# Optimization experiments

Hardware: AMD Instinct MI355X
Metric: run time of the kernel (lower is better)

Reference implementation:

```python
import jax, jax.numpy as jnp
import numpy as np

B, T, D = 2, 2048, 2048
H, KV, DH = 16, 8, 128
N, W, K = 1024, 256, 8


def rotate_half(x):
    x1, x2 = x[..., : DH // 2], x[..., DH // 2 :]
    return jnp.concatenate((-x2, x1), axis=-1)


def setup_inputs() -> dict:
    key = jax.random.key(0)
    ks = jax.random.split(key, 10)
    hidden_states = jax.random.normal(ks[0], (B, T, D), dtype=jnp.float32)
    cos = jax.random.uniform(ks[1], (B, T, DH), dtype=jnp.float32, minval=-1.0, maxval=1.0)
    sin = jax.random.uniform(ks[2], (B, T, DH), dtype=jnp.float32, minval=-1.0, maxval=1.0)
    mem = jax.random.normal(ks[3], (B, N, D), dtype=jnp.float32)
    Wq = jax.random.normal(ks[4], (D, D), dtype=jnp.float32) * 0.02
    Wk = jax.random.normal(ks[5], (KV * DH, D), dtype=jnp.float32) * 0.02
    Wv = jax.random.normal(ks[6], (KV * DH, D), dtype=jnp.float32) * 0.02
    Wo = jax.random.normal(ks[7], (D, D), dtype=jnp.float32) * 0.02
    Wg = jnp.zeros((1, D), dtype=jnp.float32)          # module inits gate weight to zeros
    bg = jnp.full((1,), 2.0, dtype=jnp.float32)        # and gate bias to 2.0
    return dict(hidden_states=hidden_states, cos=cos, sin=sin, mem=mem,
                Wq=Wq, Wk=Wk, Wv=Wv, Wo=Wo, Wg=Wg, bg=bg)


def reference(hidden_states, cos, sin, mem, Wq, Wk, Wv, Wo, Wg, bg):
    scale = DH ** -0.5
    n_rep = H // KV
    # projections -> [B, heads, T, d_h]
    q = (hidden_states @ Wq.T).reshape(B, T, H, DH).transpose(0, 2, 1, 3)
    k = (hidden_states @ Wk.T).reshape(B, T, KV, DH).transpose(0, 2, 1, 3)
    v = (hidden_states @ Wv.T).reshape(B, T, KV, DH).transpose(0, 2, 1, 3)
    # rotary (cos/sin are [B,T,d_h] -> broadcast over heads)
    c, s = cos[:, None], sin[:, None]
    q = q * c + rotate_half(q) * s
    k = k * c + rotate_half(k) * s
    # GQA repeat kv heads
    k_local = jnp.repeat(k, n_rep, axis=1)
    v_local = jnp.repeat(v, n_rep, axis=1)
    # --- local sliding-window causal attention (dense TxT mask, as in SDPA path) ---
    row = jnp.arange(T)[:, None]
    col = jnp.arange(T)[None, :]
    allowed = (col <= row) & (col >= row - W + 1)
    bias = jnp.where(allowed, 0.0, -jnp.inf).astype(q.dtype)
    scores = jnp.einsum('bhtd,bhsd->bhts', q, k_local) * scale + bias
    o_local = jnp.einsum('bhts,bhsd->bhtd', jax.nn.softmax(scores, axis=-1), v_local)
    o_local = o_local.transpose(0, 2, 1, 3).reshape(B, T, D) @ Wo.T
    # --- memory retrieval path (memory is detached in the original) ---
    mem_c = jax.lax.stop_gradient(mem)
    k_mem = (mem_c @ Wk.T).reshape(B, N, KV, DH).transpose(0, 2, 1, 3)
    v_mem = (mem_c @ Wv.T).reshape(B, N, KV, DH).transpose(0, 2, 1, 3)
    k_mem = jnp.repeat(k_mem, n_rep, axis=1)  # [B,H,N,d_h]
    v_mem = jnp.repeat(v_mem, n_rep, axis=1)
    q_chunk = q.mean(axis=2)                  # [B,H,d_h]
    sim_chunk = jnp.einsum('bhd,bhnd->bhn', q_chunk, k_mem) * scale
    _, idx = jax.lax.top_k(sim_chunk, K)      # [B,H,K]
    k_sh = jnp.take_along_axis(k_mem, idx[..., None], axis=2)  # [B,H,K,d_h]
    v_sh = jnp.take_along_axis(v_mem, idx[..., None], axis=2)
    sim_tok = jnp.einsum('bhtd,bhkd->bhtk', q, k_sh) * scale
    o_mem = jnp.einsum('bhtk,bhkd->bhtd', jax.nn.softmax(sim_tok, axis=-1), v_sh)
    o_mem = o_mem.transpose(0, 2, 1, 3).reshape(B, T, D)
    # --- learned gate fusion ---
    g = jax.nn.sigmoid(hidden_states @ Wg.T + bg)  # [B,T,1]
    return g * o_local + (1.0 - g) * o_mem
```

## Files before the change

### kernel.cpp

```cpp
#include <hip/hip_runtime.h>
#include <stdint.h>

#define B_   2
#define T_   2048
#define D_   2048
#define H_   16
#define KV_  8
#define DH_  128
#define NMEM 1024
#define WWIN 256
#define KSEL 8
#define BT   (B_*T_)
#define KVSTR 2048
#define QKVSTR 4096

__constant__ const float kScale = 0.08838834764831845f;

typedef __attribute__((ext_vector_type(8))) short s16x8;
typedef __attribute__((ext_vector_type(4))) float f32x4;

__device__ inline unsigned short f2bf(float f) {
  union { float f; unsigned int u; } c; c.f = f;
  unsigned int u = c.u;
  unsigned int r = u + 0x7fffu + ((u >> 16) & 1u);
  return (unsigned short)(r >> 16);
}
__device__ inline float bf2f(unsigned short v) {
  union { unsigned int u; float f; } c; c.u = ((unsigned int)v) << 16;
  return c.f;
}
__device__ inline f32x4 fzero4() { f32x4 v; v[0]=0.f; v[1]=0.f; v[2]=0.f; v[3]=0.f; return v; }

__global__ __launch_bounds__(256) void conv_kernel(const float* __restrict__ src,
                                                   unsigned short* __restrict__ dst, int n) {
  int i = blockIdx.x * 256 + threadIdx.x;
  if (i * 4 >= n) return;
  float4 v = ((const float4*)src)[i];
  uint2 o;
  o.x = (unsigned)f2bf(v.x) | ((unsigned)f2bf(v.y) << 16);
  o.y = (unsigned)f2bf(v.z) | ((unsigned)f2bf(v.w) << 16);
  ((uint2*)dst)[i] = o;
}

#define AOFF(buf, half) ((buf)*32768 + (half)*16384)
#define BOFF(buf, half) (65536 + (buf)*32768 + (half)*16384)

#define PH_MFMA(P, BF) \
  { \
    _Pragma("unroll") \
    for (int mi = 0; mi < 2; ++mi) { \
      _Pragma("unroll") \
      for (int ni = 0; ni < 4; ++ni) { \
        acc[P][mi][ni] = __builtin_amdgcn_mfma_f32_16x16x32_bf16(af[mi][0], BF[ni][0], acc[P][mi][ni], 0, 0, 0); \
        acc[P][mi][ni] = __builtin_amdgcn_mfma_f32_16x16x32_bf16(af[mi][1], BF[ni][1], acc[P][mi][ni], 0, 0, 0); \
      } \
    } \
  }

template<int MODE>
__global__ __launch_bounds__(512, 2) void gemm256(const unsigned short* __restrict__ A,
                                                  const unsigned short* __restrict__ Bw,
                                                  int N, int K, int lda, int ldc,
                                                  unsigned short* __restrict__ Cb,
                                                  const float* __restrict__ g,
                                                  const unsigned short* __restrict__ omem,
                                                  float* __restrict__ dout) {
  __shared__ __align__(16) char lds[131072];
  const int tid = threadIdx.x;
  const int wv = tid >> 6, lane = tid & 63;
  const int l15 = lane & 15, lg = lane >> 4;
  const int wr = wv >> 1, wc = wv & 1;
  const int gx = gridDim.x;
  const int nwg = gx * gridDim.y;
  const int flat = blockIdx.y * gx + blockIdx.x;
  const int chunk = nwg >> 3;
  const int wg = (flat & 7) * chunk + (flat >> 3);
  const int bx = wg % gx, by = wg / gx;
  const int m0 = by * 256, n0 = bx * 256;
  const int NT = K >> 6;

  auto stage_half = [&](const unsigned short* base, int stride, int row0, int koff, int ldsoff) {
#pragma unroll
    for (int ld = 0; ld < 2; ++ld) {
      int s = ld * 512 + tid;
      int row = s >> 3, cs = s & 7;
      int cg = cs ^ (row & 7);
      const unsigned short* src = base + (size_t)(row0 + row) * stride + koff + cg * 8;
      __builtin_amdgcn_global_load_lds((const __attribute__((address_space(1))) void*)src,
          (__attribute__((address_space(3))) void*)(lds + ldsoff + ld * 8192 + wv * 1024), 16, 0, 0);
    }
  };
  auto rdA = [&](int buf, int half, int mi, int kk) -> s16x8 {
    int r = wr * 32 + mi * 16 + l15;
    int slot = (kk * 4 + lg) ^ (r & 7);
    return *(const s16x8*)(lds + AOFF(buf, half) + r * 128 + slot * 16);
  };
  auto rdB = [&](int buf, int half, int ni, int kk) -> s16x8 {
    int r = wc * 64 + ni * 16 + l15;
    int slot = (kk * 4 + lg) ^ (r & 7);
    return *(const s16x8*)(lds + BOFF(buf, half) + r * 128 + slot * 16);
  };

  f32x4 acc[4][2][4];
#pragma unroll
  for (int p = 0; p < 4; ++p)
#pragma unroll
    for (int mi = 0; mi < 2; ++mi)
#pragma unroll
      for (int ni = 0; ni < 4; ++ni) acc[p][mi][ni] = fzero4();

  stage_half(A,  lda, m0,       0,  AOFF(0, 0));
  stage_half(Bw, K,   n0,       0,  BOFF(0, 0));
  stage_half(A,  lda, m0 + 128, 0,  AOFF(0, 1));
  stage_half(Bw, K,   n0 + 128, 0,  BOFF(0, 1));
  stage_half(A,  lda, m0,       64, AOFF(1, 0));
  stage_half(Bw, K,   n0,       64, BOFF(1, 0));
  stage_half(A,  lda, m0 + 128, 64, AOFF(1, 1));
  asm volatile("s_waitcnt vmcnt(6)" ::: "memory");
  __builtin_amdgcn_s_barrier();

  int cur = 0;
  for (int t = 0; t < NT; ++t, cur ^= 1) {
    const int nxt = cur ^ 1;
    s16x8 af[2][2], b0f[4][2], b1f[4][2];
#pragma unroll
    for (int mi = 0; mi < 2; ++mi) {
      af[mi][0] = rdA(cur, 0, mi, 0);
      af[mi][1] = rdA(cur, 0, mi, 1);
    }
#pragma unroll
    for (int ni = 0; ni < 4; ++ni) {
      b0f[ni][0] = rdB(cur, 0, ni, 0);
      b0f[ni][1] = rdB(cur, 0, ni, 1);
    }
    if (t + 1 < NT) stage_half(Bw, K, n0 + 128, (t + 1) * 64, BOFF(nxt, 1));
    __builtin_amdgcn_sched_barrier(0);
    __builtin_amdgcn_s_barrier();
    asm volatile("s_waitcnt lgkmcnt(0)" ::: "memory");
    __builtin_amdgcn_sched_barrier(0);
    __builtin_amdgcn_s_setprio(1);
    PH_MFMA(0, b0f);
    __builtin_amdgcn_s_setprio(0);
    __builtin_amdgcn_s_barrier();
#pragma unroll
    for (int ni = 0; ni < 4; ++ni) {
      b1f[ni][0] = rdB(cur, 1, ni, 0);
      b1f[ni][1] = rdB(cur, 1, ni, 1);
    }
    if (t + 2 < NT) stage_half(A, lda, m0, (t + 2) * 64, AOFF(cur, 0));
    __builtin_amdgcn_sched_barrier(0);
    __builtin_amdgcn_s_barrier();
    asm volatile("s_waitcnt lgkmcnt(0)" ::: "memory");
    __builtin_amdgcn_sched_barrier(0);
    __builtin_amdgcn_s_setprio(1);
    PH_MFMA(1, b1f);
    __builtin_amdgcn_s_setprio(0);
    __builtin_amdgcn_s_barrier();
#pragma unroll
    for (int mi = 0; mi < 2; ++mi) {
      af[mi][0] = rdA(cur, 1, mi, 0);
      af[mi][1] = rdA(cur, 1, mi, 1);
    }
    if (t + 2 < NT) stage_half(Bw, K, n0, (t + 2) * 64, BOFF(cur, 0));
    __builtin_amdgcn_sched_barrier(0);
    __builtin_amdgcn_s_barrier();
    asm volatile("s_waitcnt lgkmcnt(0)" ::: "memory");
    __builtin_amdgcn_sched_barrier(0);
    __builtin_amdgcn_s_setprio(1);
    PH_MFMA(2, b0f);
    __builtin_amdgcn_s_setprio(0);
    __builtin_amdgcn_s_barrier();
    if (t + 2 < NT) stage_half(A, lda, m0 + 128, (t + 2) * 64, AOFF(cur, 1));
    __builtin_amdgcn_sched_barrier(0);
    __builtin_amdgcn_s_barrier();
    __builtin_amdgcn_s_setprio(1);
    PH_MFMA(3, b1f);
    __builtin_amdgcn_s_setprio(0);
    if (t < NT - 2) asm volatile("s_waitcnt vmcnt(6)" ::: "memory");
    else            asm volatile("s_waitcnt vmcnt(0)" ::: "memory");
    __builtin_amdgcn_s_barrier();
  }

#pragma unroll
  for (int p = 0; p < 4; ++p)
#pragma unroll
    for (int mi = 0; mi < 2; ++mi)
#pragma unroll
      for (int ni = 0; ni < 4; ++ni)
#pragma unroll
        for (int j = 0; j < 4; ++j) {
          int row_g = m0 + (p >> 1) * 128 + wr * 32 + mi * 16 + lg * 4 + j;
          int col_g = n0 + (p & 1) * 128 + wc * 64 + ni * 16 + l15;
          float v = acc[p][mi][ni][j];
          size_t o = (size_t)row_g * ldc + col_g;
          if constexpr (MODE == 0) {
            Cb[o] = f2bf(v);
          } else {
            float gv = g[row_g];
            dout[o] = gv * v + (1.f - gv) * bf2f(omem[o]);
          }
        }
}

template<int MODE>
__global__ __launch_bounds__(256) void gemm_bt(const unsigned short* __restrict__ A,
                                               const unsigned short* __restrict__ Bw,
                                               int N, int K, int lda, int ldc,
                                               unsigned short* __restrict__ Cb,
                                               const float* __restrict__ g,
                                               const unsigned short* __restrict__ omem,
                                               float* __restrict__ dout) {
  __shared__ __align__(16) unsigned short sA[128 * 32];
  __shared__ __align__(16) unsigned short sB[128 * 32];
  const int tid = threadIdx.x;
  const int wv = tid >> 6, lane = tid & 63;
  const int gx = gridDim.x;
  const int nwg = gx * gridDim.y;
  const int flat = blockIdx.y * gx + blockIdx.x;
  const int chunk = nwg >> 3;
  const int wg = (flat & 7) * chunk + (flat >> 3);
  const int bx = wg % gx, by = wg / gx;
  const int m0 = by * 128, n0 = bx * 128;
  const int wr = wv >> 1, wc = wv & 1;
  const int l15 = lane & 15, lg = lane >> 4;
  const int rowA = tid >> 2;
  const int colB = (tid & 3) * 16;
  f32x4 acc[4][4];
#pragma unroll
  for (int mi = 0; mi < 4; ++mi)
#pragma unroll
    for (int ni = 0; ni < 4; ++ni) acc[mi][ni] = fzero4();

  char* sAc = (char*)sA;
  char* sBc = (char*)sB;
  for (int k0 = 0; k0 < K; k0 += 32) {
#pragma unroll
    for (int e = 0; e < 2; ++e) {
      const char* ga = (const char*)(A + ((size_t)(m0 + rowA + e * 64) * lda + k0)) + colB;
      __builtin_amdgcn_global_load_lds((const __attribute__((address_space(1))) void*)ga,
          (__attribute__((address_space(3))) void*)(sAc + e * 4096 + wv * 1024), 16, 0, 0);
      const char* gb = (const char*)(Bw + ((size_t)(n0 + rowA + e * 64) * K + k0)) + colB;
      __builtin_amdgcn_global_load_lds((const __attribute__((address_space(1))) void*)gb,
          (__attribute__((address_space(3))) void*)(sBc + e * 4096 + wv * 1024), 16, 0, 0);
    }
    __syncthreads();
    s16x8 af[4], bf_[4];
#pragma unroll
    for (int mi = 0; mi < 4; ++mi)
      af[mi] = *(const s16x8*)&sA[(wr * 64 + mi * 16 + l15) * 32 + lg * 8];
#pragma unroll
    for (int ni = 0; ni < 4; ++ni)
      bf_[ni] = *(const s16x8*)&sB[(wc * 64 + ni * 16 + l15) * 32 + lg * 8];
#pragma unroll
    for (int mi = 0; mi < 4; ++mi)
#pragma unroll
      for (int ni = 0; ni < 4; ++ni)
        acc[mi][ni] = __builtin_amdgcn_mfma_f32_16x16x32_bf16(af[mi], bf_[ni], acc[mi][ni], 0, 0, 0);
    __syncthreads();
  }
#pragma unroll
  for (int mi = 0; mi < 4; ++mi)
#pragma unroll
    for (int ni = 0; ni < 4; ++ni)
#pragma unroll
      for (int j = 0; j < 4; ++j) {
        int row_g = m0 + wr * 64 + mi * 16 + lg * 4 + j;
        int col_g = n0 + wc * 64 + ni * 16 + l15;
        float v = acc[mi][ni][j];
        size_t o = (size_t)row_g * ldc + col_g;
        if constexpr (MODE == 0) {
          Cb[o] = f2bf(v);
        } else {
          float gv = g[row_g];
          float om = bf2f(omem[o]);
          dout[o] = gv * v + (1.f - gv) * om;
        }
      }
}

__global__ __launch_bounds__(256) void rope_ip_kernel(unsigned short* __restrict__ buf,
                                                      const float* __restrict__ cosp,
                                                      const float* __restrict__ sinp,
                                                      int logp, int stride, int nthreads) {
  int i = blockIdx.x * 256 + threadIdx.x;
  if (i >= nthreads) return;
  int pp = i * 8;
  int row = pp >> logp;
  int p0 = pp & ((1 << logp) - 1);
  int blk = p0 >> 6, dd0 = p0 & 63;
  int b = row >> 11, t = row & 2047;
  const float* cb = cosp + ((size_t)b * T_ + t) * DH_;
  const float* sb = sinp + ((size_t)b * T_ + t) * DH_;
  unsigned short* p1 = buf + (size_t)row * stride + blk * 128 + dd0;
  s16x8 a = *(s16x8*)p1;
  s16x8 b8 = *(s16x8*)(p1 + 64);
  s16x8 o1, o2;
#pragma unroll
  for (int e = 0; e < 8; ++e) {
    float c1 = cb[dd0 + e], s1 = sb[dd0 + e];
    float c2 = cb[dd0 + 64 + e], s2 = sb[dd0 + 64 + e];
    float x1 = bf2f((unsigned short)a[e]), x2 = bf2f((unsigned short)b8[e]);
    o1[e] = (short)f2bf(x1 * c1 - x2 * s1);
    o2[e] = (short)f2bf(x2 * c2 + x1 * s2);
  }
  *(s16x8*)p1 = o1;
  *(s16x8*)(p1 + 64) = o2;
}

__global__ __launch_bounds__(256) void cs_kernel(const float* __restrict__ hs,
                                                 const float* __restrict__ cosp,
                                                 const float* __restrict__ sinp,
                                                 float* __restrict__ Cp, float* __restrict__ Sp) {
  __shared__ __align__(16) float hsL[32][128];
  __shared__ __align__(16) float csL[32][32];
  __shared__ __align__(16) float snL[32][32];
  const int tid = threadIdx.x;
  const int j0 = blockIdx.x * 128, d0 = blockIdx.y * 32;
  const int b = blockIdx.z >> 3, sp = blockIdx.z & 7;
  const int dq = (tid & 7) * 4;
  const int jq = (tid >> 3) * 4;
  float4 aC[4], aS[4];
#pragma unroll
  for (int a = 0; a < 4; ++a) {
    aC[a] = make_float4(0.f, 0.f, 0.f, 0.f);
    aS[a] = make_float4(0.f, 0.f, 0.f, 0.f);
  }
  const int csrow = tid >> 3, csc4 = tid & 7;
  for (int tile = 0; tile < 8; ++tile) {
    int t0 = sp * 256 + tile * 32;
    const float4* hs4 = (const float4*)(hs + ((size_t)b * T_ + t0) * D_ + j0);
#pragma unroll
    for (int r = 0; r < 4; ++r) {
      int i = tid + r * 256;
      int row = i >> 5, c4 = i & 31;
      *(float4*)&hsL[row][c4 * 4] = hs4[(size_t)row * (D_ / 4) + c4];
    }
    const float4* cp4 = (const float4*)(cosp + ((size_t)b * T_ + t0) * DH_ + d0);
    const float4* sp4 = (const float4*)(sinp + ((size_t)b * T_ + t0) * DH_ + d0);
    *(float4*)&csL[csrow][csc4 * 4] = cp4[(size_t)csrow * (DH_ / 4) + csc4];
    *(float4*)&snL[csrow][csc4 * 4] = sp4[(size_t)csrow * (DH_ / 4) + csc4];
    __syncthreads();
#pragma unroll 8
    for (int tt = 0; tt < 32; ++tt) {
      float4 cv = *(const float4*)&csL[tt][dq];
      float4 sv = *(const float4*)&snL[tt][dq];
      float4 hv = *(const float4*)&hsL[tt][jq];
      float ca[4] = {cv.x, cv.y, cv.z, cv.w};
      float sa[4] = {sv.x, sv.y, sv.z, sv.w};
#pragma unroll
      for (int a = 0; a < 4; ++a) {
        aC[a].x += ca[a] * hv.x; aC[a].y += ca[a] * hv.y;
        aC[a].z += ca[a] * hv.z; aC[a].w += ca[a] * hv.w;
        aS[a].x += sa[a] * hv.x; aS[a].y += sa[a] * hv.y;
        aS[a].z += sa[a] * hv.z; aS[a].w += sa[a] * hv.w;
      }
    }
    __syncthreads();
  }
#pragma unroll
  for (int a = 0; a < 4; ++a) {
    size_t o = ((size_t)(sp * B_ + b) * DH_ + d0 + dq + a) * D_ + j0 + jq;
    *(float4*)&Cp[o] = aC[a];
    *(float4*)&Sp[o] = aS[a];
  }
}

__global__ __launch_bounds__(256) void reduce_cs_kernel(const float4* __restrict__ Cp,
                                                        const float4* __restrict__ Sp,
                                                        float4* __restrict__ Cr,
                                                        float4* __restrict__ Sr) {
  int i = blockIdx.x * 256 + threadIdx.x;
  const int str = (B_ * DH_ * D_) / 4;
  float4 c = Cp[i], s = Sp[i];
#pragma unroll
  for (int p = 1; p < 8; ++p) {
    float4 cp = Cp[i + (size_t)p * str], sq = Sp[i + (size_t)p * str];
    c.x += cp.x; c.y += cp.y; c.z += cp.z; c.w += cp.w;
    s.x += sq.x; s.y += sq.y; s.z += sq.z; s.w += sq.w;
  }
  Cr[i] = c; Sr[i] = s;
}

__global__ __launch_bounds__(256) void qchunk_kernel(const float* __restrict__ Wq,
                                                     const float* __restrict__ Cr,
                                                     const float* __restrict__ Sr,
                                                     float* __restrict__ qc) {
  int gid = blockIdx.x * 256 + threadIdx.x;
  int wid = gid >> 6, lane = gid & 63;
  int b = wid >> 11, rem = wid & 2047;
  int h = rem >> 7, d = rem & 127;
  const float* w1 = Wq + (size_t)(h * DH_ + d) * D_;
  int dp = (d < 64) ? d + 64 : d - 64;
  float sgn = (d < 64) ? -1.f : 1.f;
  const float* w2 = Wq + (size_t)(h * DH_ + dp) * D_;
  const float* crow = Cr + ((size_t)b * DH_ + d) * D_;
  const float* srow = Sr + ((size_t)b * DH_ + d) * D_;
  float a1 = 0.f, a2 = 0.f;
  for (int j = lane; j < D_; j += 64) { a1 += w1[j] * crow[j]; a2 += w2[j] * srow[j]; }
#pragma unroll
  for (int off = 1; off < 64; off <<= 1) { a1 += __shfl_xor(a1, off); a2 += __shfl_xor(a2, off); }
  if (lane == 0) qc[wid] = (a1 + sgn * a2) * (1.f / (float)T_);
}

__global__ __launch_bounds__(256) void zk_kernel(const float* __restrict__ qc,
                                                 const float* __restrict__ Wk,
                                                 float* __restrict__ z) {
  int j = blockIdx.x * 256 + threadIdx.x;
  int h = blockIdx.y, b = blockIdx.z;
  int kvh = h >> 1;
  const float* qcl = qc + ((size_t)b * H_ + h) * DH_;
  const float* wb = Wk + (size_t)kvh * DH_ * D_ + j;
  float acc = 0.f;
#pragma unroll 8
  for (int d = 0; d < 128; ++d) acc += qcl[d] * wb[(size_t)d * D_];
  z[((size_t)b * H_ + h) * D_ + j] = acc;
}

__global__ __launch_bounds__(256) void sim_kernel(const float* __restrict__ z,
                                                  const float* __restrict__ mem,
                                                  float* __restrict__ sim) {
  __shared__ float4 mL[16 * 512];
  int tid = threadIdx.x;
  int n0 = blockIdx.x * 16, b = blockIdx.y;
  const float4* mem4 = (const float4*)(mem + (size_t)b * NMEM * D_);
#pragma unroll
  for (int c = 0; c < 32; ++c) {
    int i = tid + c * 256;
    int r = i >> 9, j4 = i & 511;
    mL[r * 512 + (j4 ^ (r & 7))] = mem4[(size_t)(n0 + r) * 512 + j4];
  }
  __syncthreads();
  int h = tid >> 4, n = tid & 15;
  const float4* zr = (const float4*)(z + ((size_t)b * H_ + h) * D_);
  float acc = 0.f;
  for (int j4 = 0; j4 < 512; ++j4) {
    float4 zz = zr[j4];
    float4 mm = mL[n * 512 + (j4 ^ (n & 7))];
    acc += zz.x * mm.x + zz.y * mm.y + zz.z * mm.z + zz.w * mm.w;
  }
  sim[((size_t)b * H_ + h) * NMEM + n0 + n] = acc * kScale;
}

__global__ __launch_bounds__(256) void topk_kernel(const float* __restrict__ sim,
                                                   int* __restrict__ idx) {
  __shared__ float sL[1024];
  __shared__ float rv[256];
  __shared__ int ri[256];
  int tid = threadIdx.x;
  int h = blockIdx.x, b = blockIdx.y;
  const float* sp = sim + ((size_t)b * H_ + h) * NMEM;
#pragma unroll
  for (int r = 0; r < 4; ++r) sL[tid + r * 256] = sp[tid + r * 256];
  __syncthreads();
  for (int kk = 0; kk < 8; ++kk) {
    float bv = -INFINITY; int bi = 0x7fffffff;
#pragma unroll
    for (int r = 0; r < 4; ++r) {
      int i = tid + r * 256;
      float v = sL[i];
      if (v > bv || (v == bv && i < bi)) { bv = v; bi = i; }
    }
    rv[tid] = bv; ri[tid] = bi;
    __syncthreads();
    for (int s = 128; s > 0; s >>= 1) {
      if (tid < s) {
        float v2 = rv[tid + s]; int i2 = ri[tid + s];
        if (v2 > rv[tid] || (v2 == rv[tid] && i2 < ri[tid])) { rv[tid] = v2; ri[tid] = i2; }
      }
      __syncthreads();
    }
    if (tid == 0) { idx[((size_t)b * H_ + h) * KSEL + kk] = ri[0]; sL[ri[0]] = -INFINITY; }
    __syncthreads();
  }
}

__global__ __launch_bounds__(256) void memattn_kernel(const unsigned short* __restrict__ qbf,
                                                      const unsigned short* __restrict__ kvmem,
                                                      const int* __restrict__ idx,
                                                      unsigned short* __restrict__ omem) {
  __shared__ float kl[8][128];
  __shared__ float vl[8][128];
  __shared__ int selL[8];
  int tid = threadIdx.x;
  int b = blockIdx.z, h = blockIdx.y, t = blockIdx.x * 256 + tid;
  int kvh = h >> 1;
  if (tid < 8) selL[tid] = idx[((size_t)b * H_ + h) * KSEL + tid];
  __syncthreads();
  {
    int r = tid >> 5, c4 = (tid & 31) * 4;
    size_t rb = ((size_t)b * NMEM + selL[r]) * (size_t)KVSTR;
    ushort4 k4 = *(const ushort4*)(kvmem + rb + kvh * DH_ + c4);
    ushort4 v4 = *(const ushort4*)(kvmem + rb + KV_ * DH_ + kvh * DH_ + c4);
    kl[r][c4 + 0] = bf2f(k4.x); kl[r][c4 + 1] = bf2f(k4.y);
    kl[r][c4 + 2] = bf2f(k4.z); kl[r][c4 + 3] = bf2f(k4.w);
    vl[r][c4 + 0] = bf2f(v4.x); vl[r][c4 + 1] = bf2f(v4.y);
    vl[r][c4 + 2] = bf2f(v4.z); vl[r][c4 + 3] = bf2f(v4.w);
  }
  __syncthreads();
  float sc[8] = {0.f,0.f,0.f,0.f,0.f,0.f,0.f,0.f};
  const unsigned short* qr = qbf + (size_t)(b * T_ + t) * QKVSTR + h * DH_;
  for (int c = 0; c < 4; ++c) {
    const s16x8* qp = (const s16x8*)(qr + c * 32);
#pragma unroll
    for (int u = 0; u < 4; ++u) {
      s16x8 q8 = qp[u];
#pragma unroll
      for (int e = 0; e < 8; ++e) {
        float qv = bf2f((unsigned short)q8[e]);
        int d = c * 32 + u * 8 + e;
#pragma unroll
        for (int kk = 0; kk < 8; ++kk) sc[kk] += qv * kl[kk][d];
      }
    }
  }
  float sm[8], mx = -INFINITY;
#pragma unroll
  for (int kk = 0; kk < 8; ++kk) { sm[kk] = sc[kk] * kScale; mx = fmaxf(mx, sm[kk]); }
  float sum = 0.f;
#pragma unroll
  for (int kk = 0; kk < 8; ++kk) { sm[kk] = __expf(sm[kk] - mx); sum += sm[kk]; }
  float inv = 1.f / sum;
#pragma unroll
  for (int kk = 0; kk < 8; ++kk) sm[kk] *= inv;
  unsigned short* orow = omem + (size_t)(b * T_ + t) * D_ + h * DH_;
  for (int d = 0; d < 128; d += 4) {
    float o0 = 0.f, o1 = 0.f, o2 = 0.f, o3 = 0.f;
#pragma unroll
    for (int kk = 0; kk < 8; ++kk) {
      float w = sm[kk];
      o0 += w * vl[kk][d + 0];
      o1 += w * vl[kk][d + 1];
      o2 += w * vl[kk][d + 2];
      o3 += w * vl[kk][d + 3];
    }
    uint2 pk;
    pk.x = (unsigned)f2bf(o0) | ((unsigned)f2bf(o1) << 16);
    pk.y = (unsigned)f2bf(o2) | ((unsigned)f2bf(o3) << 16);
    *(uint2*)(orow + d) = pk;
  }
}

__global__ __launch_bounds__(256) void gate_kernel(const float* __restrict__ hs,
                                                   const float* __restrict__ Wg,
                                                   const float* __restrict__ bg,
                                                   float* __restrict__ g) {
  int gid = blockIdx.x * 256 + threadIdx.x;
  int row = gid >> 6, lane = gid & 63;
  const float4* hr = (const float4*)(hs + (size_t)row * D_);
  const float4* wg4 = (const float4*)Wg;
  float acc = 0.f;
#pragma unroll
  for (int it = 0; it < 8; ++it) {
    float4 hv = hr[lane + it * 64], wv = wg4[lane + it * 64];
    acc += hv.x * wv.x + hv.y * wv.y + hv.z * wv.z + hv.w * wv.w;
  }
#pragma unroll
  for (int off = 1; off < 64; off <<= 1) acc += __shfl_xor(acc, off);
  if (lane == 0) g[row] = 1.f / (1.f + __expf(-(acc + bg[0])));
}

__global__ __launch_bounds__(256) void localattn_kernel(const unsigned short* __restrict__ qbf,
                                                        const unsigned short* __restrict__ kbf,
                                                        const unsigned short* __restrict__ vbf,
                                                        unsigned short* __restrict__ olocal) {
  __shared__ __align__(16) unsigned short kL[2][32][128];
  __shared__ __align__(16) unsigned short vL[2][128][32];
  __shared__ __align__(16) unsigned short pl[4][16][40];
  const int tid = threadIdx.x;
  const int w = tid >> 6, lane = tid & 63;
  const int tb = blockIdx.x * 64;
  const int h = blockIdx.y, b = blockIdx.z;
  const int kvh = h >> 1;
  const int t0 = tb + w * 16;
  const int l15 = lane & 15, lg = lane >> 4;

  s16x8 qf[4];
  {
    const unsigned short* qb = qbf + ((size_t)(b * T_ + t0 + l15) * QKVSTR) + h * DH_ + lg * 8;
#pragma unroll
    for (int kb = 0; kb < 4; ++kb) qf[kb] = *(const s16x8*)(qb + kb * 32);
  }
  f32x4 of[8];
#pragma unroll
  for (int nb = 0; nb < 8; ++nb) of[nb] = fzero4();
  float m_r[4] = {-INFINITY, -INFINITY, -INFINITY, -INFINITY};
  float l_r[4] = {0.f, 0.f, 0.f, 0.f};

  int sstart = tb - (WWIN - 1);
  if (sstart < 0) sstart = 0;
  sstart &= ~31;
  const int slast = tb + 63;

  const int vk = tid & 15, vcg = tid >> 4;
  auto STAGE = [&](int buf, int s0) {
#pragma unroll
    for (int ld = 0; ld < 2; ++ld) {
      int s = ld * 256 + tid;
      int r = s >> 4, cs = s & 15;
      int cg = cs ^ (r & 7);
      const unsigned short* src = kbf + (size_t)(b * T_ + s0 + r) * QKVSTR + kvh * DH_ + cg * 8;
      __builtin_amdgcn_global_load_lds((const __attribute__((address_space(1))) void*)src,
          (__attribute__((address_space(3))) void*)((char*)&kL[buf][0][0] + ld * 4096 + w * 1024), 16, 0, 0);
    }
    {
      int r0 = 2 * vk;
      const unsigned short* vs = vbf + (size_t)(b * T_ + s0 + r0) * QKVSTR + kvh * DH_ + vcg * 8;
      s16x8 va = *(const s16x8*)vs;
      s16x8 vb2 = *(const s16x8*)(vs + QKVSTR);
      int q = vk >> 2;
      int colbase = 2 * (vk & 3);
#pragma unroll
      for (int e = 0; e < 8; ++e) {
        int c = vcg * 8 + e;
        int blk = q ^ ((c >> 2) & 3);
        unsigned int val = (unsigned int)(unsigned short)va[e] |
                           ((unsigned int)(unsigned short)vb2[e] << 16);
        *(unsigned int*)&vL[buf][c][blk * 8 + colbase] = val;
      }
    }
  };

  STAGE(0, sstart);
  int buf = 0;
  const int vp = (l15 >> 2) & 3;
  for (int s0 = sstart; s0 <= slast; s0 += 32, buf ^= 1) {
    __syncthreads();
    if (s0 + 32 <= slast) STAGE(buf ^ 1, s0 + 32);

    f32x4 sc[2];
    sc[0] = fzero4(); sc[1] = fzero4();
#pragma unroll
    for (int cb = 0; cb < 2; ++cb) {
#pragma unroll
      for (int kb = 0; kb < 4; ++kb) {
        int r = cb * 16 + l15;
        int c = kb * 4 + lg;
        s16x8 kf = *(const s16x8*)((char*)&kL[buf][0][0] + r * 256 + ((c ^ (r & 7)) * 16));
        sc[cb] = __builtin_amdgcn_mfma_f32_16x16x32_bf16(qf[kb], kf, sc[cb], 0, 0, 0);
      }
    }
    float pv[2][4];
#pragma unroll
    for (int j = 0; j < 4; ++j) {
      int t = t0 + lg * 4 + j;
      int s_a = s0 + l15, s_b = s_a + 16;
      float va = sc[0][j] * kScale;
      float vb = sc[1][j] * kScale;
      va = (s_a <= t && s_a + (WWIN - 1) >= t) ? va : -INFINITY;
      vb = (s_b <= t && s_b + (WWIN - 1) >= t) ? vb : -INFINITY;
      float mx = fmaxf(va, vb);
#pragma unroll
      for (int off = 1; off < 16; off <<= 1) mx = fmaxf(mx, __shfl_xor(mx, off));
      float mn = fmaxf(m_r[j], mx);
      float alpha, pa, pb;
      if (mn == -INFINITY) { alpha = 1.f; pa = 0.f; pb = 0.f; }
      else {
        alpha = __expf(m_r[j] - mn);
        pa = __expf(va - mn);
        pb = __expf(vb - mn);
      }
      m_r[j] = mn;
      float rs = pa + pb;
#pragma unroll
      for (int off = 1; off < 16; off <<= 1) rs += __shfl_xor(rs, off);
      l_r[j] = l_r[j] * alpha + rs;
#pragma unroll
      for (int nb = 0; nb < 8; ++nb) of[nb][j] *= alpha;
      pv[0][j] = pa; pv[1][j] = pb;
    }
#pragma unroll
    for (int cb = 0; cb < 2; ++cb)
#pragma unroll
      for (int j = 0; j < 4; ++j)
        pl[w][lg * 4 + j][cb * 16 + l15] = f2bf(pv[cb][j]);
    asm volatile("s_waitcnt lgkmcnt(0)" ::: "memory");
    __builtin_amdgcn_sched_barrier(0);
    s16x8 pa8 = *(const s16x8*)&pl[w][l15][lg * 8];
#pragma unroll
    for (int nb = 0; nb < 8; ++nb) {
      int c = nb * 16 + l15;
      s16x8 vf = *(const s16x8*)&vL[buf][c][(lg ^ vp) * 8];
      of[nb] = __builtin_amdgcn_mfma_f32_16x16x32_bf16(pa8, vf, of[nb], 0, 0, 0);
    }
  }

  float inv[4];
#pragma unroll
  for (int j = 0; j < 4; ++j) inv[j] = 1.f / l_r[j];
#pragma unroll
  for (int nb = 0; nb < 8; ++nb)
#pragma unroll
    for (int j = 0; j < 4; ++j) {
      int t = t0 + lg * 4 + j;
      olocal[(size_t)(b * T_ + t) * QKVSTR + h * DH_ + nb * 16 + l15] = f2bf(of[nb][j] * inv[j]);
    }
}

extern "C" void kernel_launch(void* const* d_in, const int* in_sizes, int n_in,
                              void* d_out, int out_size, void* d_ws, size_t ws_size,
                              hipStream_t stream) {
  const float* hs   = (const float*)d_in[0];
  const float* cosp = (const float*)d_in[1];
  const float* sinp = (const float*)d_in[2];
  const float* mem  = (const float*)d_in[3];
  const float* Wq   = (const float*)d_in[4];
  const float* Wk   = (const float*)d_in[5];
  const float* Wv   = (const float*)d_in[6];
  const float* Wo   = (const float*)d_in[7];
  const float* Wg   = (const float*)d_in[8];
  const float* bg   = (const float*)d_in[9];
  float* out = (float*)d_out;

  char* p = (char*)d_ws;
  auto alloc = [&](size_t bytes) { char* r = p; p += (bytes + 255) & ~(size_t)255; return r; };
  float* qc     = (float*)alloc((size_t)B_ * H_ * DH_ * 4);
  float* gbuf   = (float*)alloc((size_t)BT * 4);
  float* zbuf   = (float*)alloc((size_t)B_ * H_ * D_ * 4);
  float* simbuf = (float*)alloc((size_t)B_ * H_ * NMEM * 4);
  int*   idxbuf = (int*)alloc((size_t)B_ * H_ * KSEL * 4);
  unsigned short* hs_bf   = (unsigned short*)alloc((size_t)BT * D_ * 2);
  unsigned short* qkv_raw = (unsigned short*)alloc((size_t)BT * QKVSTR * 2);
  unsigned short* wbig    = (unsigned short*)alloc((size_t)2 * D_ * D_ * 2);
  unsigned short* mem_bf  = (unsigned short*)alloc((size_t)B_ * NMEM * D_ * 2);
  unsigned short* kvmem   = (unsigned short*)alloc((size_t)B_ * NMEM * KVSTR * 2);

  float* Cp = (float*)d_out;
  float* Sp = Cp + (size_t)8 * B_ * DH_ * D_;
  float* Cr = (float*)mem_bf;
  float* Sr = Cr + (size_t)B_ * DH_ * D_;
  unsigned short* omem_bf = hs_bf;

  conv_kernel<<<(BT * D_ / 4 + 255) / 256, 256, 0, stream>>>(hs, hs_bf, BT * D_);
  conv_kernel<<<(D_ * D_ / 4 + 255) / 256, 256, 0, stream>>>(Wq, wbig, D_ * D_);
  conv_kernel<<<(KV_ * DH_ * D_ / 4 + 255) / 256, 256, 0, stream>>>(Wk, wbig + (size_t)D_ * D_, KV_ * DH_ * D_);
  conv_kernel<<<(KV_ * DH_ * D_ / 4 + 255) / 256, 256, 0, stream>>>(Wv, wbig + (size_t)D_ * D_ + (size_t)KV_ * DH_ * D_, KV_ * DH_ * D_);
  gemm256<0><<<dim3(QKVSTR / 256, BT / 256), 512, 0, stream>>>(hs_bf, wbig, QKVSTR, D_, D_, QKVSTR, qkv_raw, nullptr, nullptr, nullptr);
  conv_kernel<<<(B_ * NMEM * D_ / 4 + 255) / 256, 256, 0, stream>>>(mem, mem_bf, B_ * NMEM * D_);
  gemm_bt<0><<<dim3(KVSTR / 128, (B_ * NMEM) / 128), 256, 0, stream>>>(mem_bf, wbig + (size_t)D_ * D_, KVSTR, D_, D_, KVSTR, kvmem, nullptr, nullptr, nullptr);

  rope_ip_kernel<<<(BT * D_ / 16 + 255) / 256, 256, 0, stream>>>(qkv_raw, cosp, sinp, 10, QKVSTR, BT * D_ / 16);
  rope_ip_kernel<<<(BT * KV_ * DH_ / 16 + 255) / 256, 256, 0, stream>>>(qkv_raw + D_, cosp, sinp, 9, QKVSTR, BT * KV_ * DH_ / 16);

  cs_kernel<<<dim3(D_ / 128, DH_ / 32, B_ * 8), 256, 0, stream>>>(hs, cosp, sinp, Cp, Sp);
  reduce_cs_kernel<<<(B_ * DH_ * D_ / 4) / 256, 256, 0, stream>>>((const float4*)Cp, (const float4*)Sp, (float4*)Cr, (float4*)Sr);
  qchunk_kernel<<<(B_ * H_ * DH_) / 4, 256, 0, stream>>>(Wq, Cr, Sr, qc);
  zk_kernel<<<dim3(D_ / 256, H_, B_), 256, 0, stream>>>(qc, Wk, zbuf);
  sim_kernel<<<dim3(NMEM / 16, B_), 256, 0, stream>>>(zbuf, mem, simbuf);
  topk_kernel<<<dim3(H_, B_), 256, 0, stream>>>(simbuf, idxbuf);

  memattn_kernel<<<dim3(T_ / 256, H_, B_), 256, 0, stream>>>(qkv_raw, kvmem, idxbuf, omem_bf);

  gate_kernel<<<BT / 4, 256, 0, stream>>>(hs, Wg, bg, gbuf);

  localattn_kernel<<<dim3(T_ / 64, H_, B_), 256, 0, stream>>>(qkv_raw, qkv_raw + D_, qkv_raw + D_ + KV_ * DH_, qkv_raw);

  conv_kernel<<<(D_ * D_ / 4 + 255) / 256, 256, 0, stream>>>(Wo, wbig, D_ * D_);
  gemm256<1><<<dim3(D_ / 256, BT / 256), 512, 0, stream>>>(qkv_raw, wbig, D_, D_, QKVSTR, D_, nullptr, gbuf, omem_bf, out);
}
```

Baseline: 437.2 us.

## Merge memory K/V projection into the main QKV GEMM via stacked rows

Stacks the bf16 hidden states and memory rows into one A buffer and runs a single 256-tile GEMM producing Q, K and V for both, removing the separate 128-tile gemm_bt launch for memory K/V. Memory attention now reads selected K/V rows from the combined output buffer. This removes one kernel launch and uses the larger-tile GEMM for the memory projection, but computes an unneeded Q projection for memory rows, adding GEMM work and output traffic.

```diff
diff --git a/kernel.cpp b/kernel.cpp
--- a/kernel.cpp
+++ b/kernel.cpp
@@ -11,8 +11,8 @@
 #define WWIN 256
 #define KSEL 8
 #define BT   (B_*T_)
-#define KVSTR 2048
 #define QKVSTR 4096
+#define MROWS (BT + B_*NMEM)
 
 __constant__ const float kScale = 0.08838834764831845f;
 
@@ -202,82 +202,6 @@
         }
 }
 
-template<int MODE>
-__global__ __launch_bounds__(256) void gemm_bt(const unsigned short* __restrict__ A,
-                                               const unsigned short* __restrict__ Bw,
-                                               int N, int K, int lda, int ldc,
-                                               unsigned short* __restrict__ Cb,
-                                               const float* __restrict__ g,
-                                               const unsigned short* __restrict__ omem,
-                                               float* __restrict__ dout) {
-  __shared__ __align__(16) unsigned short sA[128 * 32];
-  __shared__ __align__(16) unsigned short sB[128 * 32];
-  const int tid = threadIdx.x;
-  const int wv = tid >> 6, lane = tid & 63;
-  const int gx = gridDim.x;
-  const int nwg = gx * gridDim.y;
-  const int flat = blockIdx.y * gx + blockIdx.x;
-  const int chunk = nwg >> 3;
-  const int wg = (flat & 7) * chunk + (flat >> 3);
-  const int bx = wg % gx, by = wg / gx;
-  const int m0 = by * 128, n0 = bx * 128;
-  const int wr = wv >> 1, wc = wv & 1;
-  const int l15 = lane & 15, lg = lane >> 4;
-  const int rowA = tid >> 2;
-  const int colB = (tid & 3) * 16;
-  f32x4 acc[4][4];
-#pragma unroll
-  for (int mi = 0; mi < 4; ++mi)
-#pragma unroll
-    for (int ni = 0; ni < 4; ++ni) acc[mi][ni] = fzero4();
-
-  char* sAc = (char*)sA;
-  char* sBc = (char*)sB;
-  for (int k0 = 0; k0 < K; k0 += 32) {
-#pragma unroll
-    for (int e = 0; e < 2; ++e) {
-      const char* ga = (const char*)(A + ((size_t)(m0 + rowA + e * 64) * lda + k0)) + colB;
-      __builtin_amdgcn_global_load_lds((const __attribute__((address_space(1))) void*)ga,
-          (__attribute__((address_space(3))) void*)(sAc + e * 4096 + wv * 1024), 16, 0, 0);
-      const char* gb = (const char*)(Bw + ((size_t)(n0 + rowA + e * 64) * K + k0)) + colB;
-      __builtin_amdgcn_global_load_lds((const __attribute__((address_space(1))) void*)gb,
-          (__attribute__((address_space(3))) void*)(sBc + e * 4096 + wv * 1024), 16, 0, 0);
-    }
-    __syncthreads();
-    s16x8 af[4], bf_[4];
-#pragma unroll
-    for (int mi = 0; mi < 4; ++mi)
-      af[mi] = *(const s16x8*)&sA[(wr * 64 + mi * 16 + l15) * 32 + lg * 8];
-#pragma unroll
-    for (int ni = 0; ni < 4; ++ni)
-      bf_[ni] = *(const s16x8*)&sB[(wc * 64 + ni * 16 + l15) * 32 + lg * 8];
-#pragma unroll
-    for (int mi = 0; mi < 4; ++mi)
-#pragma unroll
-      for (int ni = 0; ni < 4; ++ni)
-        acc[mi][ni] = __builtin_amdgcn_mfma_f32_16x16x32_bf16(af[mi], bf_[ni], acc[mi][ni], 0, 0, 0);
-    __syncthreads();
-  }
-#pragma unroll
-  for (int mi = 0; mi < 4; ++mi)
-#pragma unroll
-    for (int ni = 0; ni < 4; ++ni)
-#pragma unroll
-      for (int j = 0; j < 4; ++j) {
-        int row_g = m0 + wr * 64 + mi * 16 + lg * 4 + j;
-        int col_g = n0 + wc * 64 + ni * 16 + l15;
-        float v = acc[mi][ni][j];
-        size_t o = (size_t)row_g * ldc + col_g;
-        if constexpr (MODE == 0) {
-          Cb[o] = f2bf(v);
-        } else {
-          float gv = g[row_g];
-          float om = bf2f(omem[o]);
-          dout[o] = gv * v + (1.f - gv) * om;
-        }
-      }
-}
-
 __global__ __launch_bounds__(256) void rope_ip_kernel(unsigned short* __restrict__ buf,
                                                       const float* __restrict__ cosp,
                                                       const float* __restrict__ sinp,
@@ -475,7 +399,7 @@
 }
 
 __global__ __launch_bounds__(256) void memattn_kernel(const unsigned short* __restrict__ qbf,
-                                                      const unsigned short* __restrict__ kvmem,
+                                                      const unsigned short* __restrict__ qkvm,
                                                       const int* __restrict__ idx,
                                                       unsigned short* __restrict__ omem) {
   __shared__ float kl[8][128];
@@ -488,9 +412,9 @@
   __syncthreads();
   {
     int r = tid >> 5, c4 = (tid & 31) * 4;
-    size_t rb = ((size_t)b * NMEM + selL[r]) * (size_t)KVSTR;
-    ushort4 k4 = *(const ushort4*)(kvmem + rb + kvh * DH_ + c4);
-    ushort4 v4 = *(const ushort4*)(kvmem + rb + KV_ * DH_ + kvh * DH_ + c4);
+    size_t rb = ((size_t)(BT + b * NMEM + selL[r])) * (size_t)QKVSTR;
+    ushort4 k4 = *(const ushort4*)(qkvm + rb + D_ + kvh * DH_ + c4);
+    ushort4 v4 = *(const ushort4*)(qkvm + rb + D_ + KV_ * DH_ + kvh * DH_ + c4);
     kl[r][c4 + 0] = bf2f(k4.x); kl[r][c4 + 1] = bf2f(k4.y);
     kl[r][c4 + 2] = bf2f(k4.z); kl[r][c4 + 3] = bf2f(k4.w);
     vl[r][c4 + 0] = bf2f(v4.x); vl[r][c4 + 1] = bf2f(v4.y);
@@ -718,28 +642,27 @@
   float* zbuf   = (float*)alloc((size_t)B_ * H_ * D_ * 4);
   float* simbuf = (float*)alloc((size_t)B_ * H_ * NMEM * 4);
   int*   idxbuf = (int*)alloc((size_t)B_ * H_ * KSEL * 4);
-  unsigned short* hs_bf   = (unsigned short*)alloc((size_t)BT * D_ * 2);
-  unsigned short* qkv_raw = (unsigned short*)alloc((size_t)BT * QKVSTR * 2);
-  unsigned short* wbig    = (unsigned short*)alloc((size_t)2 * D_ * D_ * 2);
-  unsigned short* mem_bf  = (unsigned short*)alloc((size_t)B_ * NMEM * D_ * 2);
-  unsigned short* kvmem   = (unsigned short*)alloc((size_t)B_ * NMEM * KVSTR * 2);
-
+  unsigned short* Abuf  = (unsigned short*)alloc((size_t)MROWS * D_ * 2);
+  unsigned short* qkvm  = (unsigned short*)alloc((size_t)MROWS * QKVSTR * 2);
+  unsigned short* wbig  = (unsigned short*)alloc((size_t)2 * D_ * D_ * 2);
+
+  unsigned short* hs_bf  = Abuf;
+  unsigned short* mem_bf = Abuf + (size_t)BT * D_;
   float* Cp = (float*)d_out;
   float* Sp = Cp + (size_t)8 * B_ * DH_ * D_;
-  float* Cr = (float*)mem_bf;
+  float* Cr = (float*)Abuf;
   float* Sr = Cr + (size_t)B_ * DH_ * D_;
-  unsigned short* omem_bf = hs_bf;
+  unsigned short* omem_bf = Abuf;
 
   conv_kernel<<<(BT * D_ / 4 + 255) / 256, 256, 0, stream>>>(hs, hs_bf, BT * D_);
+  conv_kernel<<<(B_ * NMEM * D_ / 4 + 255) / 256, 256, 0, stream>>>(mem, mem_bf, B_ * NMEM * D_);
   conv_kernel<<<(D_ * D_ / 4 + 255) / 256, 256, 0, stream>>>(Wq, wbig, D_ * D_);
   conv_kernel<<<(KV_ * DH_ * D_ / 4 + 255) / 256, 256, 0, stream>>>(Wk, wbig + (size_t)D_ * D_, KV_ * DH_ * D_);
   conv_kernel<<<(KV_ * DH_ * D_ / 4 + 255) / 256, 256, 0, stream>>>(Wv, wbig + (size_t)D_ * D_ + (size_t)KV_ * DH_ * D_, KV_ * DH_ * D_);
-  gemm256<0><<<dim3(QKVSTR / 256, BT / 256), 512, 0, stream>>>(hs_bf, wbig, QKVSTR, D_, D_, QKVSTR, qkv_raw, nullptr, nullptr, nullptr);
-  conv_kernel<<<(B_ * NMEM * D_ / 4 + 255) / 256, 256, 0, stream>>>(mem, mem_bf, B_ * NMEM * D_);
-  gemm_bt<0><<<dim3(KVSTR / 128, (B_ * NMEM) / 128), 256, 0, stream>>>(mem_bf, wbig + (size_t)D_ * D_, KVSTR, D_, D_, KVSTR, kvmem, nullptr, nullptr, nullptr);
-
-  rope_ip_kernel<<<(BT * D_ / 16 + 255) / 256, 256, 0, stream>>>(qkv_raw, cosp, sinp, 10, QKVSTR, BT * D_ / 16);
-  rope_ip_kernel<<<(BT * KV_ * DH_ / 16 + 255) / 256, 256, 0, stream>>>(qkv_raw + D_, cosp, sinp, 9, QKVSTR, BT * KV_ * DH_ / 16);
+  gemm256<0><<<dim3(QKVSTR / 256, MROWS / 256), 512, 0, stream>>>(Abuf, wbig, QKVSTR, D_, D_, QKVSTR, qkvm, nullptr, nullptr, nullptr);
+
+  rope_ip_kernel<<<(BT * D_ / 16 + 255) / 256, 256, 0, stream>>>(qkvm, cosp, sinp, 10, QKVSTR, BT * D_ / 16);
+  rope_ip_kernel<<<(BT * KV_ * DH_ / 16 + 255) / 256, 256, 0, stream>>>(qkvm + D_, cosp, sinp, 9, QKVSTR, BT * KV_ * DH_ / 16);
 
   cs_kernel<<<dim3(D_ / 128, DH_ / 32, B_ * 8), 256, 0, stream>>>(hs, cosp, sinp, Cp, Sp);
   reduce_cs_kernel<<<(B_ * DH_ * D_ / 4) / 256, 256, 0, stream>>>((const float4*)Cp, (const float4*)Sp, (float4*)Cr, (float4*)Sr);
@@ -748,12 +671,12 @@
   sim_kernel<<<dim3(NMEM / 16, B_), 256, 0, stream>>>(zbuf, mem, simbuf);
   topk_kernel<<<dim3(H_, B_), 256, 0, stream>>>(simbuf, idxbuf);
 
-  memattn_kernel<<<dim3(T_ / 256, H_, B_), 256, 0, stream>>>(qkv_raw, kvmem, idxbuf, omem_bf);
+  memattn_kernel<<<dim3(T_ / 256, H_, B_), 256, 0, stream>>>(qkvm, qkvm, idxbuf, omem_bf);
 
   gate_kernel<<<BT / 4, 256, 0, stream>>>(hs, Wg, bg, gbuf);
 
-  localattn_kernel<<<dim3(T_ / 64, H_, B_), 256, 0, stream>>>(qkv_raw, qkv_raw + D_, qkv_raw + D_ + KV_ * DH_, qkv_raw);
+  localattn_kernel<<<dim3(T_ / 64, H_, B_), 256, 0, stream>>>(qkvm, qkvm + D_, qkvm + D_ + KV_ * DH_, qkvm);
 
   conv_kernel<<<(D_ * D_ / 4 + 255) / 256, 256, 0, stream>>>(Wo, wbig, D_ * D_);
-  gemm256<1><<<dim3(D_ / 256, BT / 256), 512, 0, stream>>>(qkv_raw, wbig, D_, D_, QKVSTR, D_, nullptr, gbuf, omem_bf, out);
-}
+  gemm256<1><<<dim3(D_ / 256, BT / 256), 512, 0, stream>>>(qkvm, wbig, D_, D_, QKVSTR, D_, nullptr, gbuf, omem_bf, out);
+}
```

After: 447.1 us. +2.3%, slower.
